# Kernel tuning notes

Hardware: AMD Instinct MI355X
Metric: run time of the kernel (lower is better)

## Reference

```python
import jax, jax.numpy as jnp
import numpy as np

INPUT, EMB, HID, FC1 = 15, 32, 128, 64


def _lstm_layer(x, W_ih, W_hh, b_ih, b_hh):
    """Single unidirectional LSTM layer, batch_first input x: (B, T, D).
    Returns (outputs (B,T,H), last hidden (B,H)). PyTorch gate order i,f,g,o."""
    B, T, _ = x.shape
    H = W_hh.shape[1]
    # Precompute input projections for all timesteps in one big GEMM.
    xg = jnp.einsum('btd,gd->btg', x, W_ih) + b_ih + b_hh  # (B, T, 4H)
    xg = jnp.transpose(xg, (1, 0, 2))  # (T, B, 4H) for scan

    def step(carry, g_t):
        h, c = carry
        g = g_t + h @ W_hh.T  # (B, 4H)
        i = jax.nn.sigmoid(g[:, :H])
        f = jax.nn.sigmoid(g[:, H:2 * H])
        gg = jnp.tanh(g[:, 2 * H:3 * H])
        o = jax.nn.sigmoid(g[:, 3 * H:])
        c = f * c + i * gg
        h = o * jnp.tanh(c)
        return (h, c), h

    h0 = jnp.zeros((B, H), dtype=x.dtype)
    c0 = jnp.zeros((B, H), dtype=x.dtype)
    (h_last, _), outs = jax.lax.scan(step, (h0, c0), xg)
    return jnp.transpose(outs, (1, 0, 2)), h_last


def setup_inputs() -> dict:
    key = jax.random.key(0)
    ks = jax.random.split(key, 12)
    B, T = 2048, 576
    s_emb = 1.0 / np.sqrt(INPUT)
    s0 = 1.0 / np.sqrt(HID)
    s_fc1 = 1.0 / np.sqrt(HID)
    s_fc2 = 1.0 / np.sqrt(FC1)
    return {
        'x': jax.random.normal(ks[0], (B, T, INPUT), jnp.float32),
        'W_emb': jax.random.uniform(ks[1], (EMB, INPUT), jnp.float32, -s_emb, s_emb),
        'b_emb': jax.random.uniform(ks[2], (EMB,), jnp.float32, -s_emb, s_emb),
        'W_ih0': jax.random.uniform(ks[3], (4 * HID, EMB), jnp.float32, -s0, s0),
        'W_hh0': jax.random.uniform(ks[4], (4 * HID, HID), jnp.float32, -s0, s0),
        'b_ih0': jax.random.uniform(ks[5], (4 * HID,), jnp.float32, -s0, s0),
        'b_hh0': jax.random.uniform(ks[6], (4 * HID,), jnp.float32, -s0, s0),
        'W_ih1': jax.random.uniform(ks[7], (4 * HID, HID), jnp.float32, -s0, s0),
        'W_hh1': jax.random.uniform(ks[8], (4 * HID, HID), jnp.float32, -s0, s0),
        'b_ih1': jax.random.uniform(ks[9], (4 * HID,), jnp.float32, -s0, s0),
        'b_hh1': jax.random.uniform(ks[10], (4 * HID,), jnp.float32, -s0, s0),
        'W_fc1': jax.random.uniform(ks[11], (FC1, HID), jnp.float32, -s_fc1, s_fc1),
        'b_fc1': jnp.zeros((FC1,), jnp.float32),
        'W_fc2': jax.random.uniform(jax.random.fold_in(key, 99), (1, FC1), jnp.float32, -s_fc2, s_fc2),
        'b_fc2': jnp.zeros((1,), jnp.float32),
    }


def reference(x, W_emb, b_emb, W_ih0, W_hh0, b_ih0, b_hh0,
              W_ih1, W_hh1, b_ih1, b_hh1, W_fc1, b_fc1, W_fc2, b_fc2):
    # Linear embedding: 15 -> 32
    e = jnp.einsum('bti,ei->bte', x, W_emb) + b_emb
    # 2-layer LSTM (eval mode -> inter-layer dropout disabled)
    out0, _ = _lstm_layer(e, W_ih0, W_hh0, b_ih0, b_hh0)
    _, h_last = _lstm_layer(out0, W_ih1, W_hh1, b_ih1, b_hh1)  # (B, HID)
    # FC head: 128 -> 64 -> 1 (eval mode dropout disabled)
    z = jax.nn.relu(h_last @ W_fc1.T + b_fc1)
    logits = z @ W_fc2.T + b_fc2  # (B, 1)
    return logits
```

## Files before the change

kernel.cpp:

```cpp
#include <hip/hip_runtime.h>

#define TS    576
#define TC    288
#define HID   128
#define GT    512
#define K0P   160
#define BB    8
#define NT    1024
#define BNT   256
#define BROWS 32
#define TS128 (TS*HID)

__device__ float g_wt0[K0P * GT];
__device__ float g_b0[GT];
__device__ float g_wih1[HID * GT];
__device__ float g_whh1[HID * GT];
__device__ float g_b1[GT];
__device__ float g_out0[(size_t)2048 * TS * HID];
__device__ float g_G1[(size_t)2048 * TC * GT];
__device__ float g_h1[2048 * HID];
__device__ float g_c1[2048 * HID];

__global__ void prep_kernel(const float* __restrict__ W_emb, const float* __restrict__ b_emb,
                            const float* __restrict__ W_ih0, const float* __restrict__ W_hh0,
                            const float* __restrict__ b_ih0, const float* __restrict__ b_hh0,
                            const float* __restrict__ W_ih1, const float* __restrict__ W_hh1,
                            const float* __restrict__ b_ih1, const float* __restrict__ b_hh1)
{
    const int jo = blockIdx.x * blockDim.x + threadIdx.x;
    if (jo >= GT) return;
    const int g  = jo >> 7;
    const int u  = jo & 127;
    const int jn = (u << 2) | g;

    for (int i = 0; i < 15; ++i) {
        float s = 0.f;
        for (int c = 0; c < 32; ++c) s = fmaf(W_ih0[jo*32 + c], W_emb[c*15 + i], s);
        g_wt0[i*GT + jn] = s;
    }
    for (int k = 0; k < HID; ++k) g_wt0[(15 + k)*GT + jn] = W_hh0[jo*HID + k];
    for (int k = 143; k < K0P; ++k) g_wt0[k*GT + jn] = 0.f;
    float bb = b_ih0[jo] + b_hh0[jo];
    for (int c = 0; c < 32; ++c) bb = fmaf(W_ih0[jo*32 + c], b_emb[c], bb);
    g_b0[jn] = bb;

    for (int k = 0; k < HID; ++k) g_wih1[k*GT + jn] = W_ih1[jo*HID + k];
    for (int k = 0; k < HID; ++k) g_whh1[k*GT + jn] = W_hh1[jo*HID + k];
    g_b1[jn] = b_ih1[jo] + b_hh1[jo];
}

__device__ __forceinline__ float sigm(float v)   { return __builtin_amdgcn_rcpf(1.f + __expf(-v)); }
__device__ __forceinline__ float tanh_f(float v) { return 1.f - 2.f * __builtin_amdgcn_rcpf(1.f + __expf(2.f * v)); }

#define LD4(P_) (*(const float4*)(P_))
#define FMARC(A_, SV_, W_) \
    A_.x = fmaf(SV_, W_.x, A_.x); A_.y = fmaf(SV_, W_.y, A_.y); \
    A_.z = fmaf(SV_, W_.z, A_.z); A_.w = fmaf(SV_, W_.w, A_.w);

__global__ void __attribute__((amdgpu_flat_work_group_size(NT, NT)))
lstm_l0(const float* __restrict__ x, float* __restrict__ out0)
{
    __shared__ float src0[BB][K0P];
    __shared__ float part[8][BB][GT];

    const int tid  = threadIdx.x;
    const int cg   = tid & 127;
    const int q4   = cg << 2;
    const int ks   = tid >> 7;
    const int um   = cg;
    const int ur   = tid >> 7;
    const int row0 = blockIdx.x * BB;
    const int k0b  = ks * 20;

    const float* p0 = g_wt0 + (size_t)k0b * GT + q4;
#define DECLA(I_) const float4 wa##I_ = LD4(p0 + (I_)*GT);
    DECLA(0)  DECLA(1)  DECLA(2)  DECLA(3)  DECLA(4)
    DECLA(5)  DECLA(6)  DECLA(7)  DECLA(8)  DECLA(9)
    DECLA(10) DECLA(11) DECLA(12) DECLA(13) DECLA(14)
    DECLA(15) DECLA(16) DECLA(17) DECLA(18) DECLA(19)

    const float4 zz = make_float4(0.f, 0.f, 0.f, 0.f);
    const float4 i0 = (ks == 0) ? LD4(g_b0 + q4) : zz;
    float c0 = 0.f;

    for (int i = tid; i < BB*K0P; i += NT) (&src0[0][0])[i] = 0.f;

    const int lr = tid / 15, li = tid - lr * 15;
    const float* xp = x + (size_t)(row0 + (tid < 120 ? lr : 0)) * (TS * 15) + (tid < 120 ? li : 0);

    __syncthreads();
    if (tid < 120) src0[lr][li] = xp[0];
    __syncthreads();

    float* pp = &part[ks][0][0];

#define L0R(R_) { \
    const float* sp_ = &src0[R_][k0b]; \
    const float4 s0_ = LD4(sp_+0),  s1_ = LD4(sp_+4),  s2_ = LD4(sp_+8); \
    const float4 s3_ = LD4(sp_+12), s4_ = LD4(sp_+16); \
    float4 acc_ = i0; \
    FMARC(acc_, s0_.x, wa0)  FMARC(acc_, s0_.y, wa1)  FMARC(acc_, s0_.z, wa2)  FMARC(acc_, s0_.w, wa3)  \
    FMARC(acc_, s1_.x, wa4)  FMARC(acc_, s1_.y, wa5)  FMARC(acc_, s1_.z, wa6)  FMARC(acc_, s1_.w, wa7)  \
    FMARC(acc_, s2_.x, wa8)  FMARC(acc_, s2_.y, wa9)  FMARC(acc_, s2_.z, wa10) FMARC(acc_, s2_.w, wa11) \
    FMARC(acc_, s3_.x, wa12) FMARC(acc_, s3_.y, wa13) FMARC(acc_, s3_.z, wa14) FMARC(acc_, s3_.w, wa15) \
    FMARC(acc_, s4_.x, wa16) FMARC(acc_, s4_.y, wa17) FMARC(acc_, s4_.z, wa18) FMARC(acc_, s4_.w, wa19) \
    *(float4*)(pp + (R_)*GT + q4) = acc_; }

    #pragma unroll 1
    for (int t = 0; t < TS; ++t) {
        float xnext = 0.f;
        if (tid < 120 && t + 1 < TS) xnext = xp[(size_t)(t + 1) * 15];
        L0R(0) L0R(1) L0R(2) L0R(3) L0R(4) L0R(5) L0R(6) L0R(7)
        __syncthreads();
        {
            const int ub = um << 2;
            float4 gv = LD4(&part[0][ur][ub]);
            #pragma unroll
            for (int s = 1; s < 8; ++s) {
                const float4 p = LD4(&part[s][ur][ub]);
                gv.x += p.x; gv.y += p.y; gv.z += p.z; gv.w += p.w;
            }
            const float iv = sigm(gv.x), fv = sigm(gv.y), ov = sigm(gv.w);
            const float gg = tanh_f(gv.z);
            c0 = fmaf(fv, c0, iv * gg);
            const float hv = ov * tanh_f(c0);
            src0[ur][15 + um] = hv;
            out0[(size_t)(row0 + ur) * TS128 + (size_t)t * HID + um] = hv;
        }
        if (tid < 120 && t + 1 < TS) src0[lr][li] = xnext;
        __syncthreads();
    }
}

__global__ void __launch_bounds__(BNT)
proj1(int t0)
{
    __shared__ float At[HID][36];

    const int tid = threadIdx.x;
    const int rb  = blockIdx.x * BROWS;

    {
        const int row = tid >> 3;
        const int g   = rb + row;
        const int b   = g / TC;
        const int tc  = g - b * TC;
        const float* src = g_out0 + (size_t)(b * TS + t0 + tc) * HID;
        #pragma unroll
        for (int i = 0; i < 4; ++i) {
            const int kq = (tid & 7) + 8 * i;
            const float4 v = LD4(src + kq * 4);
            At[kq*4 + 0][row] = v.x;
            At[kq*4 + 1][row] = v.y;
            At[kq*4 + 2][row] = v.z;
            At[kq*4 + 3][row] = v.w;
        }
    }
    __syncthreads();

    const int q  = tid & 127;
    const int r0 = (tid >> 7) * 16;
    const float4 bq = LD4(g_b1 + q * 4);
    float4 a0=bq,a1=bq,a2=bq,a3=bq,a4=bq,a5=bq,a6=bq,a7=bq;
    float4 a8=bq,a9=bq,a10=bq,a11=bq,a12=bq,a13=bq,a14=bq,a15=bq;

    const float* wp = g_wih1 + q * 4;
    #pragma unroll 4
    for (int k = 0; k < HID; ++k) {
        const float4 wv = LD4(wp + (size_t)k * GT);
        const float4 h0_ = LD4(&At[k][r0 + 0]);
        const float4 h1_ = LD4(&At[k][r0 + 4]);
        const float4 h2_ = LD4(&At[k][r0 + 8]);
        const float4 h3_ = LD4(&At[k][r0 + 12]);
        FMARC(a0,  h0_.x, wv) FMARC(a1,  h0_.y, wv) FMARC(a2,  h0_.z, wv) FMARC(a3,  h0_.w, wv)
        FMARC(a4,  h1_.x, wv) FMARC(a5,  h1_.y, wv) FMARC(a6,  h1_.z, wv) FMARC(a7,  h1_.w, wv)
        FMARC(a8,  h2_.x, wv) FMARC(a9,  h2_.y, wv) FMARC(a10, h2_.z, wv) FMARC(a11, h2_.w, wv)
        FMARC(a12, h3_.x, wv) FMARC(a13, h3_.y, wv) FMARC(a14, h3_.z, wv) FMARC(a15, h3_.w, wv)
    }

    float* dst = g_G1 + (size_t)(rb + r0) * GT + q * 4;
#define STG(I_) *(float4*)(dst + (size_t)(I_) * GT) = a##I_;
    STG(0) STG(1) STG(2) STG(3) STG(4) STG(5) STG(6) STG(7)
    STG(8) STG(9) STG(10) STG(11) STG(12) STG(13) STG(14) STG(15)
}

__global__ void __attribute__((amdgpu_flat_work_group_size(NT, NT)))
lstm_l1(int t0, int last,
        const float* __restrict__ W_fc1, const float* __restrict__ b_fc1,
        const float* __restrict__ W_fc2, const float* __restrict__ b_fc2,
        float* __restrict__ out)
{
    __shared__ float h1s[BB][HID];
    __shared__ float obuf[BB][GT];
    __shared__ float part[8][BB][GT];

    const int tid  = threadIdx.x;
    const int cg   = tid & 127;
    const int q4   = cg << 2;
    const int ks   = tid >> 7;
    const int um   = cg;
    const int ur   = tid >> 7;
    const int row0 = blockIdx.x * BB;
    const int k1b  = ks * 16;

    const float* ph = g_whh1 + (size_t)k1b * GT + q4;
#define DECLB(I_) const float4 wb##I_ = LD4(ph + (I_)*GT);
    DECLB(0)  DECLB(1)  DECLB(2)  DECLB(3)
    DECLB(4)  DECLB(5)  DECLB(6)  DECLB(7)
    DECLB(8)  DECLB(9)  DECLB(10) DECLB(11)
    DECLB(12) DECLB(13) DECLB(14) DECLB(15)

    const float4 zz = make_float4(0.f, 0.f, 0.f, 0.f);
    float c1;

    if (t0 == 0) {
        h1s[ur][um] = 0.f;
        c1 = 0.f;
    } else {
        h1s[ur][um] = g_h1[(row0 + ur) * HID + um];
        c1 = g_c1[(row0 + ur) * HID + um];
    }

    const int pr = tid >> 7, pq = tid & 127;
    const float* gp = g_G1 + ((size_t)(row0 + pr) * TC) * GT + pq * 4;
    float4 pf = LD4(gp);
    __syncthreads();
    *(float4*)(&obuf[pr][pq << 2]) = pf;
    __syncthreads();

    float* pp = &part[ks][0][0];

#define L1R(R_) { \
    const float4 h0_ = LD4(&h1s[R_][k1b + 0]); \
    const float4 h1_ = LD4(&h1s[R_][k1b + 4]); \
    const float4 h2_ = LD4(&h1s[R_][k1b + 8]); \
    const float4 h3_ = LD4(&h1s[R_][k1b + 12]); \
    float4 acc_ = (ks == 0) ? LD4(&obuf[R_][q4]) : zz; \
    FMARC(acc_, h0_.x, wb0)  FMARC(acc_, h0_.y, wb1)  FMARC(acc_, h0_.z, wb2)  FMARC(acc_, h0_.w, wb3)  \
    FMARC(acc_, h1_.x, wb4)  FMARC(acc_, h1_.y, wb5)  FMARC(acc_, h1_.z, wb6)  FMARC(acc_, h1_.w, wb7)  \
    FMARC(acc_, h2_.x, wb8)  FMARC(acc_, h2_.y, wb9)  FMARC(acc_, h2_.z, wb10) FMARC(acc_, h2_.w, wb11) \
    FMARC(acc_, h3_.x, wb12) FMARC(acc_, h3_.y, wb13) FMARC(acc_, h3_.z, wb14) FMARC(acc_, h3_.w, wb15) \
    *(float4*)(pp + (R_)*GT + q4) = acc_; }

    #pragma unroll 1
    for (int tc = 0; tc < TC; ++tc) {
        L1R(0) L1R(1) L1R(2) L1R(3) L1R(4) L1R(5) L1R(6) L1R(7)
        if (tc + 1 < TC) pf = LD4(gp + (size_t)(tc + 1) * GT);
        __syncthreads();
        {
            const int ub = um << 2;
            float4 gv = LD4(&part[0][ur][ub]);
            #pragma unroll
            for (int s = 1; s < 8; ++s) {
                const float4 p = LD4(&part[s][ur][ub]);
                gv.x += p.x; gv.y += p.y; gv.z += p.z; gv.w += p.w;
            }
            const float iv = sigm(gv.x), fv = sigm(gv.y), ov = sigm(gv.w);
            const float gg = tanh_f(gv.z);
            c1 = fmaf(fv, c1, iv * gg);
            h1s[ur][um] = ov * tanh_f(c1);
        }
        if (tc + 1 < TC) *(float4*)(&obuf[pr][pq << 2]) = pf;
        __syncthreads();
    }

    g_h1[(row0 + ur) * HID + um] = h1s[ur][um];
    g_c1[(row0 + ur) * HID + um] = c1;

    if (last) {
        if (tid < BB * 64) {
            const int rr = tid >> 6, u = tid & 63;
            float acc = b_fc1[u];
            #pragma unroll 8
            for (int k = 0; k < HID; ++k) acc = fmaf(h1s[rr][k], W_fc1[u*HID + k], acc);
            part[0][rr][u] = fmaxf(acc, 0.f);
        }
        __syncthreads();
        if (tid < BB) {
            float acc = b_fc2[0];
            #pragma unroll 8
            for (int u = 0; u < 64; ++u) acc = fmaf(part[0][tid][u], W_fc2[u], acc);
            out[row0 + tid] = acc;
        }
    }
}

extern "C" void kernel_launch(void* const* d_in, const int* in_sizes, int n_in,
                              void* d_out, int out_size, void* d_ws, size_t ws_size,
                              hipStream_t stream)
{
    const float* x     = (const float*)d_in[0];
    const float* W_emb = (const float*)d_in[1];
    const float* b_emb = (const float*)d_in[2];
    const float* W_ih0 = (const float*)d_in[3];
    const float* W_hh0 = (const float*)d_in[4];
    const float* b_ih0 = (const float*)d_in[5];
    const float* b_hh0 = (const float*)d_in[6];
    const float* W_ih1 = (const float*)d_in[7];
    const float* W_hh1 = (const float*)d_in[8];
    const float* b_ih1 = (const float*)d_in[9];
    const float* b_hh1 = (const float*)d_in[10];
    const float* W_fc1 = (const float*)d_in[11];
    const float* b_fc1 = (const float*)d_in[12];
    const float* W_fc2 = (const float*)d_in[13];
    const float* b_fc2 = (const float*)d_in[14];
    float* out = (float*)d_out;

    float* out0;
    hipGetSymbolAddress((void**)&out0, HIP_SYMBOL(g_out0));

    prep_kernel<<<2, 256, 0, stream>>>(W_emb, b_emb, W_ih0, W_hh0, b_ih0, b_hh0,
                                       W_ih1, W_hh1, b_ih1, b_hh1);
    lstm_l0<<<2048 / BB, NT, 0, stream>>>(x, out0);

    const int projBlocks = 2048 * TC / BROWS;
    for (int c = 0; c < TS / TC; ++c) {
        proj1<<<projBlocks, BNT, 0, stream>>>(c * TC);
        lstm_l1<<<2048 / BB, NT, 0, stream>>>(c * TC, (c == TS / TC - 1) ? 1 : 0,
                                              W_fc1, b_fc1, W_fc2, b_fc2, out);
    }
}
```

Baseline: 6.554 ms.

## Split LSTM batch rows into two halves to overlap gate updates with matvec

```diff
diff --git a/kernel.cpp b/kernel.cpp
--- a/kernel.cpp
+++ b/kernel.cpp
@@ -67,8 +67,6 @@
     const int cg   = tid & 127;
     const int q4   = cg << 2;
     const int ks   = tid >> 7;
-    const int um   = cg;
-    const int ur   = tid >> 7;
     const int row0 = blockIdx.x * BB;
     const int k0b  = ks * 20;
 
@@ -81,15 +79,20 @@
 
     const float4 zz = make_float4(0.f, 0.f, 0.f, 0.f);
     const float4 i0 = (ks == 0) ? LD4(g_b0 + q4) : zz;
-    float c0 = 0.f;
+
+    const int ur4 = (tid >> 7) & 3;
+    const int um  = tid & 127;
+    float c_lo = 0.f, c_hi = 0.f;
+
+    const bool xs = (tid >= 512 && tid < 572);
+    const int  sx  = xs ? (tid - 512) : 0;
+    const int  lr4 = sx / 15, li = sx - lr4 * 15;
+    const float* xpl = x + (size_t)(row0 + lr4)     * (TS * 15) + li;
+    const float* xph = x + (size_t)(row0 + 4 + lr4) * (TS * 15) + li;
 
     for (int i = tid; i < BB*K0P; i += NT) (&src0[0][0])[i] = 0.f;
-
-    const int lr = tid / 15, li = tid - lr * 15;
-    const float* xp = x + (size_t)(row0 + (tid < 120 ? lr : 0)) * (TS * 15) + (tid < 120 ? li : 0);
-
-    __syncthreads();
-    if (tid < 120) src0[lr][li] = xp[0];
+    __syncthreads();
+    if (xs) src0[lr4][li] = xpl[0];
     __syncthreads();
 
     float* pp = &part[ks][0][0];
@@ -106,30 +109,33 @@
     FMARC(acc_, s4_.x, wa16) FMARC(acc_, s4_.y, wa17) FMARC(acc_, s4_.z, wa18) FMARC(acc_, s4_.w, wa19) \
     *(float4*)(pp + (R_)*GT + q4) = acc_; }
 
+#define UPD0(ROW_, C_, TU_) { \
+    const int ub_ = um << 2; \
+    float4 gv_ = LD4(&part[0][ROW_][ub_]); \
+    _Pragma("unroll") \
+    for (int s_ = 1; s_ < 8; ++s_) { \
+        const float4 p_ = LD4(&part[s_][ROW_][ub_]); \
+        gv_.x += p_.x; gv_.y += p_.y; gv_.z += p_.z; gv_.w += p_.w; \
+    } \
+    const float iv_ = sigm(gv_.x), fv_ = sigm(gv_.y), ov_ = sigm(gv_.w); \
+    const float gg_ = tanh_f(gv_.z); \
+    C_ = fmaf(fv_, C_, iv_ * gg_); \
+    const float hv_ = ov_ * tanh_f(C_); \
+    src0[ROW_][15 + um] = hv_; \
+    out0[(size_t)(row0 + (ROW_)) * TS128 + (size_t)(TU_) * HID + um] = hv_; }
+
     #pragma unroll 1
     for (int t = 0; t < TS; ++t) {
-        float xnext = 0.f;
-        if (tid < 120 && t + 1 < TS) xnext = xp[(size_t)(t + 1) * 15];
-        L0R(0) L0R(1) L0R(2) L0R(3) L0R(4) L0R(5) L0R(6) L0R(7)
-        __syncthreads();
-        {
-            const int ub = um << 2;
-            float4 gv = LD4(&part[0][ur][ub]);
-            #pragma unroll
-            for (int s = 1; s < 8; ++s) {
-                const float4 p = LD4(&part[s][ur][ub]);
-                gv.x += p.x; gv.y += p.y; gv.z += p.z; gv.w += p.w;
-            }
-            const float iv = sigm(gv.x), fv = sigm(gv.y), ov = sigm(gv.w);
-            const float gg = tanh_f(gv.z);
-            c0 = fmaf(fv, c0, iv * gg);
-            const float hv = ov * tanh_f(c0);
-            src0[ur][15 + um] = hv;
-            out0[(size_t)(row0 + ur) * TS128 + (size_t)t * HID + um] = hv;
-        }
-        if (tid < 120 && t + 1 < TS) src0[lr][li] = xnext;
-        __syncthreads();
-    }
+        L0R(0) L0R(1) L0R(2) L0R(3)
+        if (tid < 512) { if (t > 0) UPD0(4 + ur4, c_hi, t - 1) }
+        else if (xs)   src0[4 + lr4][li] = xph[(size_t)t * 15];
+        __syncthreads();
+        L0R(4) L0R(5) L0R(6) L0R(7)
+        if (tid < 512) { UPD0(ur4, c_lo, t) }
+        else if (xs && t + 1 < TS) src0[lr4][li] = xpl[(size_t)(t + 1) * 15];
+        __syncthreads();
+    }
+    if (tid < 512) UPD0(4 + ur4, c_hi, TS - 1)
 }
 
 __global__ void __launch_bounds__(BNT)
@@ -198,8 +204,6 @@
     const int cg   = tid & 127;
     const int q4   = cg << 2;
     const int ks   = tid >> 7;
-    const int um   = cg;
-    const int ur   = tid >> 7;
     const int row0 = blockIdx.x * BB;
     const int k1b  = ks * 16;
 
@@ -211,21 +215,27 @@
     DECLB(12) DECLB(13) DECLB(14) DECLB(15)
 
     const float4 zz = make_float4(0.f, 0.f, 0.f, 0.f);
-    float c1;
+
+    const int ur4 = (tid >> 7) & 3;
+    const int um  = tid & 127;
+    float c_lo, c_hi;
+
+    const int pr4 = (tid >> 7) & 3;
+    const int pq  = tid & 127;
+    const float* gpl = g_G1 + ((size_t)(row0 + pr4)     * TC) * GT + pq * 4;
+    const float* gph = g_G1 + ((size_t)(row0 + 4 + pr4) * TC) * GT + pq * 4;
 
     if (t0 == 0) {
-        h1s[ur][um] = 0.f;
-        c1 = 0.f;
+        c_lo = 0.f; c_hi = 0.f;
+        h1s[tid >> 7][um] = 0.f;
+        if (tid >= 512) h1s[4 + pr4][pq] = 0.f;
     } else {
-        h1s[ur][um] = g_h1[(row0 + ur) * HID + um];
-        c1 = g_c1[(row0 + ur) * HID + um];
-    }
-
-    const int pr = tid >> 7, pq = tid & 127;
-    const float* gp = g_G1 + ((size_t)(row0 + pr) * TC) * GT + pq * 4;
-    float4 pf = LD4(gp);
-    __syncthreads();
-    *(float4*)(&obuf[pr][pq << 2]) = pf;
+        h1s[tid >> 7][um] = g_h1[(row0 + (tid >> 7)) * HID + um];
+        c_lo = g_c1[(row0 + ur4) * HID + um];
+        c_hi = g_c1[(row0 + 4 + ur4) * HID + um];
+    }
+    __syncthreads();
+    if (tid >= 512) *(float4*)(&obuf[pr4][pq << 2]) = LD4(gpl);
     __syncthreads();
 
     float* pp = &part[ks][0][0];
@@ -242,30 +252,38 @@
     FMARC(acc_, h3_.x, wb12) FMARC(acc_, h3_.y, wb13) FMARC(acc_, h3_.z, wb14) FMARC(acc_, h3_.w, wb15) \
     *(float4*)(pp + (R_)*GT + q4) = acc_; }
 
+#define UPD1(ROW_, C_) { \
+    const int ub_ = um << 2; \
+    float4 gv_ = LD4(&part[0][ROW_][ub_]); \
+    _Pragma("unroll") \
+    for (int s_ = 1; s_ < 8; ++s_) { \
+        const float4 p_ = LD4(&part[s_][ROW_][ub_]); \
+        gv_.x += p_.x; gv_.y += p_.y; gv_.z += p_.z; gv_.w += p_.w; \
+    } \
+    const float iv_ = sigm(gv_.x), fv_ = sigm(gv_.y), ov_ = sigm(gv_.w); \
+    const float gg_ = tanh_f(gv_.z); \
+    C_ = fmaf(fv_, C_, iv_ * gg_); \
+    h1s[ROW_][um] = ov_ * tanh_f(C_); }
+
     #pragma unroll 1
-    for (int tc = 0; tc < TC; ++tc) {
-        L1R(0) L1R(1) L1R(2) L1R(3) L1R(4) L1R(5) L1R(6) L1R(7)
-        if (tc + 1 < TC) pf = LD4(gp + (size_t)(tc + 1) * GT);
-        __syncthreads();
-        {
-            const int ub = um << 2;
-            float4 gv = LD4(&part[0][ur][ub]);
-            #pragma unroll
-            for (int s = 1; s < 8; ++s) {
-                const float4 p = LD4(&part[s][ur][ub]);
-                gv.x += p.x; gv.y += p.y; gv.z += p.z; gv.w += p.w;
-            }
-            const float iv = sigm(gv.x), fv = sigm(gv.y), ov = sigm(gv.w);
-            const float gg = tanh_f(gv.z);
-            c1 = fmaf(fv, c1, iv * gg);
-            h1s[ur][um] = ov * tanh_f(c1);
-        }
-        if (tc + 1 < TC) *(float4*)(&obuf[pr][pq << 2]) = pf;
-        __syncthreads();
-    }
-
-    g_h1[(row0 + ur) * HID + um] = h1s[ur][um];
-    g_c1[(row0 + ur) * HID + um] = c1;
+    for (int t = 0; t < TC; ++t) {
+        L1R(0) L1R(1) L1R(2) L1R(3)
+        if (tid < 512) { if (t > 0) UPD1(4 + ur4, c_hi) }
+        else *(float4*)(&obuf[4 + pr4][pq << 2]) = LD4(gph + (size_t)t * GT);
+        __syncthreads();
+        L1R(4) L1R(5) L1R(6) L1R(7)
+        if (tid < 512) { UPD1(ur4, c_lo) }
+        else if (t + 1 < TC) *(float4*)(&obuf[pr4][pq << 2]) = LD4(gpl + (size_t)(t + 1) * GT);
+        __syncthreads();
+    }
+    if (tid < 512) UPD1(4 + ur4, c_hi)
+    __syncthreads();
+
+    g_h1[(row0 + (tid >> 7)) * HID + um] = h1s[tid >> 7][um];
+    if (tid < 512) {
+        g_c1[(row0 + ur4) * HID + um]     = c_lo;
+        g_c1[(row0 + 4 + ur4) * HID + um] = c_hi;
+    }
 
     if (last) {
         if (tid < BB * 64) {
```

After: 6.760 ms. 3.1% more time.
